# Kernel optimization log

Measured on AMD Instinct MI355X. Metric: run time of the kernel, lower is better.

The kernel has to match this reference:

```python
import jax, jax.numpy as jnp
import numpy as np

ATOM_FDIM = 133
BOND_FDIM = 147
HIDDEN = 300
DEPTH = 3
N_ATOMS = 100000
N_BONDS = 200000
MAX_NB = 6
N_MOLS = 4000


def setup_inputs() -> dict:
    key = jax.random.key(0)
    ks = jax.random.split(key, 10)
    f_atoms = jax.random.normal(ks[0], (N_ATOMS, ATOM_FDIM), dtype=jnp.float32)
    f_bonds = jax.random.normal(ks[1], (N_BONDS, BOND_FDIM), dtype=jnp.float32)
    a2b = jax.random.randint(ks[2], (N_ATOMS, MAX_NB), 0, N_BONDS)
    b2a = jax.random.randint(ks[3], (N_BONDS,), 0, N_ATOMS)
    b2revb = jax.random.randint(ks[4], (N_BONDS,), 0, N_BONDS)
    atom2mol = jnp.sort(jax.random.randint(ks[5], (N_ATOMS,), 0, N_MOLS))
    s = 1.0 / np.sqrt(HIDDEN)
    W_i = jax.random.uniform(ks[6], (BOND_FDIM, HIDDEN), jnp.float32, -s, s)
    W_h = jax.random.uniform(ks[7], (HIDDEN, HIDDEN), jnp.float32, -s, s)
    W_o_w = jax.random.uniform(ks[8], (ATOM_FDIM + HIDDEN, HIDDEN), jnp.float32, -s, s)
    W_o_b = jax.random.uniform(ks[9], (HIDDEN,), jnp.float32, -s, s)
    return {"f_atoms": f_atoms, "f_bonds": f_bonds, "a2b": a2b, "b2a": b2a,
            "b2revb": b2revb, "atom2mol": atom2mol, "W_i": W_i, "W_h": W_h,
            "W_o_w": W_o_w, "W_o_b": W_o_b}


def reference(f_atoms, f_bonds, a2b, b2a, b2revb, atom2mol, W_i, W_h, W_o_w, W_o_b):
    # input = W_i(f_bonds); message = act(input)
    inp = f_bonds @ W_i                      # [n_bonds, hidden]
    message = jax.nn.relu(inp)
    for _ in range(DEPTH - 1):
        # gather neighbor bond messages per atom and sum: [n_atoms, max_nb, h] -> [n_atoms, h]
        a_message = message[a2b].sum(axis=1)
        rev_message = message[b2revb]        # [n_bonds, hidden]
        message = a_message[b2a] - rev_message
        message = jax.nn.relu(inp + message @ W_h)
    # final atom-level aggregation
    a_message = message[a2b].sum(axis=1)     # [n_atoms, hidden]
    a_input = jnp.concatenate([f_atoms, a_message], axis=1)
    atom_hiddens = jax.nn.relu(a_input @ W_o_w + W_o_b)
    # segment mean pooling over molecules
    sums = jax.ops.segment_sum(atom_hiddens, atom2mol, num_segments=N_MOLS)
    counts = jax.ops.segment_sum(jnp.ones((atom_hiddens.shape[0],), atom_hiddens.dtype),
                                 atom2mol, num_segments=N_MOLS)
    mol_vecs = sums / jnp.maximum(counts, 1.0)[:, None]  # zero vec for empty mols
    return mol_vecs
```

## Files before the change

### kernel.cpp

```cpp
#include <hip/hip_runtime.h>
#include <stdint.h>

#define ATOM_FDIM 133
#define BOND_FDIM 147
#define HIDDEN    300
#define N_ATOMS   100000
#define N_BONDS   200000
#define MAX_NB    6
#define N_MOLS    4000

#define KP_I 160
#define KP_H 320
#define KP_O 448
#define LDA  304
#define CPR  38

#define TM   128
#define ACH  8
#define BCH  20

typedef unsigned short u16;
typedef short bf16x8 __attribute__((ext_vector_type(8)));
typedef float f32x4 __attribute__((ext_vector_type(4)));

__device__ __forceinline__ u16 f2bu(float f) {
    unsigned u = __float_as_uint(f);
    u += 0x7FFFu + ((u >> 16) & 1u);
    return (u16)(u >> 16);
}
__device__ __forceinline__ float bu2f(u16 b) { return __uint_as_float(((unsigned)b) << 16); }

__device__ __forceinline__ uint4 relu_bf16x8(uint4 v) {
    union { uint4 u; u16 s[8]; } x, o;
    x.u = v;
    #pragma unroll
    for (int e = 0; e < 8; ++e) o.s[e] = (x.s[e] & 0x8000u) ? (u16)0 : x.s[e];
    return o.u;
}
__device__ __forceinline__ uint4 comb_bf16x8(uint4 vi, uint4 va, uint4 vy) {
    union { uint4 u; u16 s[8]; } xi, xa, xy, o;
    xi.u = vi; xa.u = va; xy.u = vy;
    #pragma unroll
    for (int e = 0; e < 8; ++e)
        o.s[e] = f2bu(fmaxf(bu2f(xi.s[e]) + bu2f(xa.s[e]) - bu2f(xy.s[e]), 0.f));
    return o.u;
}

#define AS1 __attribute__((address_space(1)))
#define AS3 __attribute__((address_space(3)))
__device__ __forceinline__ void gl_lds(const void* g, void* l) {
    __builtin_amdgcn_global_load_lds((const AS1 void*)g, (AS3 void*)l, 16, 0, 0);
}

template <int EPI>
__global__ __launch_bounds__(512, 2) void mm_k(
    const u16* __restrict__ A, int lda,
    const u16* __restrict__ Wp,
    const float* __restrict__ bias,
    u16* __restrict__ out0, int ldo0,
    int M, int NT)
{
    __shared__ __align__(16) u16 As[3][ACH * 512];
    __shared__ __align__(16) u16 Bs[3][BCH * 512];

    const int t    = threadIdx.x;
    const int lane = t & 63, wid = t >> 6;
    const int fl   = lane & 15, fh = lane >> 4;
    const int m0   = blockIdx.x * TM;
    const int wr   = wid >> 1, wc = wid & 1;

    int arow = m0 + wid * 16 + fl;
    if (arow > M - 1) arow = M - 1;
    const char* srcAp = (const char*)A + (size_t)arow * (size_t)lda * 2u + (size_t)(fh * 16);
    const char* WpC = (const char*)Wp;
    const int bbase = (wid < 4) ? 3 * wid : 12 + 2 * (wid - 4);
    const size_t srcB0 = (size_t)bbase * 1024u + (size_t)lane * 16u;

    f32x4 acc[2][10] = {};

#define STAGE_T(kt, buf) do {                                                    \
        const size_t kbB_ = (size_t)(kt) * (size_t)(BCH * 1024);                 \
        gl_lds(srcAp + (size_t)(kt) * 64u, (char*)As[buf] + wid * 1024);         \
        gl_lds(WpC + kbB_ + srcB0,        (char*)Bs[buf] + bbase * 1024);        \
        gl_lds(WpC + kbB_ + srcB0 + 1024, (char*)Bs[buf] + bbase * 1024 + 1024); \
        if (wid < 4)                                                             \
            gl_lds(WpC + kbB_ + srcB0 + 2048, (char*)Bs[buf] + bbase * 1024 + 2048); \
    } while (0)

#define GATE() do {                                                        \
        if (wid < 4) asm volatile("s_waitcnt vmcnt(4)" ::: "memory");      \
        else         asm volatile("s_waitcnt vmcnt(3)" ::: "memory");      \
    } while (0)

    STAGE_T(0, 0);
    STAGE_T(1, 1);
    GATE();
    __builtin_amdgcn_s_barrier();

    int cur = 0;
    for (int tt = 0; tt < NT; ++tt) {
        int w2 = tt + 2; if (w2 >= NT) w2 -= NT;
        const int nx1 = (cur < 2) ? cur + 1 : 0;
        const int nx2 = (nx1 < 2) ? nx1 + 1 : 0;
        const u16* as_c = As[cur];
        const u16* bs_c = Bs[cur];
        const size_t kbB = (size_t)w2 * (size_t)(BCH * 1024);

        bf16x8 af0, af1, bfv[10];
        af0 = *reinterpret_cast<const bf16x8*>(&as_c[(wr * 2 + 0) * 512 + lane * 8]);
        af1 = *reinterpret_cast<const bf16x8*>(&as_c[(wr * 2 + 1) * 512 + lane * 8]);
        #pragma unroll
        for (int n = 0; n < 5; ++n)
            bfv[n] = *reinterpret_cast<const bf16x8*>(&bs_c[(wc * 10 + n) * 512 + lane * 8]);
        gl_lds(srcAp + (size_t)w2 * 64u, (char*)As[nx2] + wid * 1024);
        gl_lds(WpC + kbB + srcB0, (char*)Bs[nx2] + bbase * 1024);
        __builtin_amdgcn_s_barrier();
        __builtin_amdgcn_s_setprio(1);
        #pragma unroll
        for (int n = 0; n < 5; ++n) {
            acc[0][n] = __builtin_amdgcn_mfma_f32_16x16x32_bf16(af0, bfv[n], acc[0][n], 0, 0, 0);
            acc[1][n] = __builtin_amdgcn_mfma_f32_16x16x32_bf16(af1, bfv[n], acc[1][n], 0, 0, 0);
        }
        __builtin_amdgcn_s_setprio(0);
        __builtin_amdgcn_s_barrier();

        #pragma unroll
        for (int n = 5; n < 10; ++n)
            bfv[n] = *reinterpret_cast<const bf16x8*>(&bs_c[(wc * 10 + n) * 512 + lane * 8]);
        gl_lds(WpC + kbB + srcB0 + 1024, (char*)Bs[nx2] + bbase * 1024 + 1024);
        if (wid < 4)
            gl_lds(WpC + kbB + srcB0 + 2048, (char*)Bs[nx2] + bbase * 1024 + 2048);
        GATE();
        __builtin_amdgcn_s_barrier();
        __builtin_amdgcn_s_setprio(1);
        #pragma unroll
        for (int n = 5; n < 10; ++n) {
            acc[0][n] = __builtin_amdgcn_mfma_f32_16x16x32_bf16(af0, bfv[n], acc[0][n], 0, 0, 0);
            acc[1][n] = __builtin_amdgcn_mfma_f32_16x16x32_bf16(af1, bfv[n], acc[1][n], 0, 0, 0);
        }
        __builtin_amdgcn_s_setprio(0);
        __builtin_amdgcn_s_barrier();
        cur = nx1;
    }
#undef STAGE_T
#undef GATE

    #pragma unroll
    for (int m = 0; m < 2; ++m) {
        #pragma unroll
        for (int r = 0; r < 4; ++r) {
            const int row = m0 + wr * 32 + m * 16 + fh * 4 + r;
            if (row >= M) continue;
            #pragma unroll
            for (int n = 0; n < 10; ++n) {
                const int col = wc * 160 + n * 16 + fl;
                if (col >= HIDDEN) continue;
                const float v = acc[m][n][r];
                if (EPI == 1) out0[(size_t)row * ldo0 + col] = f2bu(v);
                else          out0[(size_t)row * ldo0 + col] = f2bu(fmaxf(v + bias[col], 0.f));
            }
        }
    }
}

template <int AM>
__global__ __launch_bounds__(512, 2) void mmf_k(
    const u16* __restrict__ A, int lda,
    const u16* __restrict__ aYp,
    const u16* __restrict__ Yp,
    const int* __restrict__ b2a,
    const int* __restrict__ b2revb,
    const u16* __restrict__ Wp,
    u16* __restrict__ out0, int ldo0,
    int M, int NT)
{
    __shared__ __align__(16) u16 As[2][ACH * 512];
    __shared__ __align__(16) u16 Bs[3][BCH * 512];

    const int t    = threadIdx.x;
    const int lane = t & 63, wid = t >> 6;
    const int fl   = lane & 15, fh = lane >> 4;
    const int m0   = blockIdx.x * TM;
    const int wr   = wid >> 1, wc = wid & 1;

    int arow = m0 + wid * 16 + fl;
    if (arow > M - 1) arow = M - 1;
    const char* pI = (const char*)A + (size_t)arow * (size_t)lda * 2u + (size_t)(fh * 16);
    const char* pA = nullptr; const char* pY = nullptr;
    if constexpr (AM == 2) {
        const int ia = b2a[arow], ir = b2revb[arow];
        pA = (const char*)aYp + (size_t)ia * (LDA * 2) + (size_t)(fh * 16);
        pY = (const char*)Yp  + (size_t)ir * (LDA * 2) + (size_t)(fh * 16);
    }
    const char* WpC = (const char*)Wp;
    const int bbase = (wid < 4) ? 3 * wid : 12 + 2 * (wid - 4);
    const size_t srcB0 = (size_t)bbase * 1024u + (size_t)lane * 16u;

    f32x4 acc[2][10] = {};
    uint4 Xi, Xa, Xy, Yi, Ya, Yy;
    (void)Xa; (void)Xy; (void)Ya; (void)Yy;

    Xi = *reinterpret_cast<const uint4*>(pI);
    if constexpr (AM == 2) { Xa = *reinterpret_cast<const uint4*>(pA);
                             Xy = *reinterpret_cast<const uint4*>(pY); }
    gl_lds(WpC + srcB0, (char*)Bs[0] + bbase * 1024);
    gl_lds(WpC + srcB0 + 1024, (char*)Bs[0] + bbase * 1024 + 1024);
    if (wid < 4) gl_lds(WpC + srcB0 + 2048, (char*)Bs[0] + bbase * 1024 + 2048);
    Yi = *reinterpret_cast<const uint4*>(pI + 64);
    if constexpr (AM == 2) { Ya = *reinterpret_cast<const uint4*>(pA + 64);
                             Yy = *reinterpret_cast<const uint4*>(pY + 64); }
    {
        const size_t kb1 = (size_t)(BCH * 1024);
        gl_lds(WpC + kb1 + srcB0, (char*)Bs[1] + bbase * 1024);
        gl_lds(WpC + kb1 + srcB0 + 1024, (char*)Bs[1] + bbase * 1024 + 1024);
        if (wid < 4) gl_lds(WpC + kb1 + srcB0 + 2048, (char*)Bs[1] + bbase * 1024 + 2048);
    }
    if constexpr (AM == 2) {
        if (wid < 4) asm volatile("s_waitcnt vmcnt(9)" ::: "memory");
        else         asm volatile("s_waitcnt vmcnt(7)" ::: "memory");
    } else {
        if (wid < 4) asm volatile("s_waitcnt vmcnt(7)" ::: "memory");
        else         asm volatile("s_waitcnt vmcnt(5)" ::: "memory");
    }
    {
        uint4 w0;
        if constexpr (AM == 2) w0 = comb_bf16x8(Xi, Xa, Xy);
        else                   w0 = relu_bf16x8(Xi);
        *reinterpret_cast<uint4*>(&As[0][wid * 512 + lane * 8]) = w0;
    }
    if constexpr (AM == 2) {
        if (wid < 4) asm volatile("s_waitcnt vmcnt(6)" ::: "memory");
        else         asm volatile("s_waitcnt vmcnt(5)" ::: "memory");
    } else {
        if (wid < 4) asm volatile("s_waitcnt vmcnt(4)" ::: "memory");
        else         asm volatile("s_waitcnt vmcnt(3)" ::: "memory");
    }
    asm volatile("s_waitcnt lgkmcnt(0)" ::: "memory");
    __builtin_amdgcn_s_barrier();

    int tt = 0, bcur = 0;

#define GATE() do {                                                        \
    if constexpr (AM == 2) {                                               \
        if (wid < 4) asm volatile("s_waitcnt vmcnt(6)" ::: "memory");      \
        else         asm volatile("s_waitcnt vmcnt(5)" ::: "memory");      \
    } else {                                                               \
        if (wid < 4) asm volatile("s_waitcnt vmcnt(4)" ::: "memory");      \
        else         asm volatile("s_waitcnt vmcnt(3)" ::: "memory");      \
    } } while (0)

#define STEP(LI, LA, LY, WI, WA, WY) do {                                                   \
    int w2 = tt + 2; if (w2 >= NT) w2 -= NT;                                                \
    const u16* as_c = As[tt & 1];                                                           \
    const u16* bs_c = Bs[bcur];                                                             \
    int bnx = bcur + 2; if (bnx >= 3) bnx -= 3;                                             \
    char* bdst = (char*)Bs[bnx] + bbase * 1024;                                             \
    const size_t kbB = (size_t)w2 * (size_t)(BCH * 1024);                                   \
    bf16x8 af0, af1, bfv[10];                                                               \
    af0 = *reinterpret_cast<const bf16x8*>(&as_c[(wr * 2 + 0) * 512 + lane * 8]);           \
    af1 = *reinterpret_cast<const bf16x8*>(&as_c[(wr * 2 + 1) * 512 + lane * 8]);           \
    _Pragma("unroll")                                                                       \
    for (int n = 0; n < 5; ++n)                                                             \
        bfv[n] = *reinterpret_cast<const bf16x8*>(&bs_c[(wc * 10 + n) * 512 + lane * 8]);   \
    LI = *reinterpret_cast<const uint4*>(pI + (size_t)w2 * 64u);                            \
    if constexpr (AM == 2) {                                                                \
        LA = *reinterpret_cast<const uint4*>(pA + (size_t)w2 * 64u);                        \
        LY = *reinterpret_cast<const uint4*>(pY + (size_t)w2 * 64u);                        \
    }                                                                                       \
    gl_lds(WpC + kbB + srcB0, bdst);                                                        \
    __builtin_amdgcn_s_barrier();                                                           \
    __builtin_amdgcn_s_setprio(1);                                                          \
    _Pragma("unroll")                                                                       \
    for (int n = 0; n < 5; ++n) {                                                           \
        acc[0][n] = __builtin_amdgcn_mfma_f32_16x16x32_bf16(af0, bfv[n], acc[0][n], 0,0,0); \
        acc[1][n] = __builtin_amdgcn_mfma_f32_16x16x32_bf16(af1, bfv[n], acc[1][n], 0,0,0); \
    }                                                                                       \
    __builtin_amdgcn_s_setprio(0);                                                          \
    __builtin_amdgcn_s_barrier();                                                           \
    _Pragma("unroll")                                                                       \
    for (int n = 5; n < 10; ++n)                                                            \
        bfv[n] = *reinterpret_cast<const bf16x8*>(&bs_c[(wc * 10 + n) * 512 + lane * 8]);   \
    gl_lds(WpC + kbB + srcB0 + 1024, bdst + 1024);                                          \
    if (wid < 4) gl_lds(WpC + kbB + srcB0 + 2048, bdst + 2048);                             \
    GATE();                                                                                 \
    {                                                                                       \
        uint4 wv;                                                                           \
        if constexpr (AM == 2) wv = comb_bf16x8(WI, WA, WY);                                \
        else                   wv = relu_bf16x8(WI);                                        \
        *reinterpret_cast<uint4*>(&As[(tt + 1) & 1][wid * 512 + lane * 8]) = wv;            \
    }                                                                                       \
    asm volatile("s_waitcnt lgkmcnt(0)" ::: "memory");                                      \
    __builtin_amdgcn_s_barrier();                                                           \
    __builtin_amdgcn_s_setprio(1);                                                          \
    _Pragma("unroll")                                                                       \
    for (int n = 5; n < 10; ++n) {                                                          \
        acc[0][n] = __builtin_amdgcn_mfma_f32_16x16x32_bf16(af0, bfv[n], acc[0][n], 0,0,0); \
        acc[1][n] = __builtin_amdgcn_mfma_f32_16x16x32_bf16(af1, bfv[n], acc[1][n], 0,0,0); \
    }                                                                                       \
    __builtin_amdgcn_s_setprio(0);                                                          \
    __builtin_amdgcn_s_barrier();                                                           \
    ++tt; bcur = (bcur == 2) ? 0 : bcur + 1;                                                \
} while (0)

    while (tt + 1 < NT) {
        STEP(Xi, Xa, Xy, Yi, Ya, Yy);
        STEP(Yi, Ya, Yy, Xi, Xa, Xy);
    }
    if (tt < NT) STEP(Xi, Xa, Xy, Yi, Ya, Yy);
#undef STEP
#undef GATE

    #pragma unroll
    for (int m = 0; m < 2; ++m) {
        #pragma unroll
        for (int r = 0; r < 4; ++r) {
            const int row = m0 + wr * 32 + m * 16 + fh * 4 + r;
            if (row >= M) continue;
            #pragma unroll
            for (int n = 0; n < 10; ++n) {
                const int col = wc * 160 + n * 16 + fl;
                if (col >= HIDDEN) continue;
                out0[(size_t)row * ldo0 + col] = f2bu(acc[m][n][r]);
            }
        }
    }
}

__global__ __launch_bounds__(256) void wconv_k(const float* __restrict__ W,
                                               int split, int off1, int Ktot, int NT,
                                               u16* __restrict__ Wp)
{
    const int id = blockIdx.x * 256 + threadIdx.x;
    if (id >= NT * BCH * 512) return;
    const int block = id >> 9, rem = id & 511;
    const int l = rem >> 3, e = rem & 7;
    const int c = block % BCH, kt = block / BCH;
    const int col = c * 16 + (l & 15);
    const int k   = kt * 32 + (l >> 4) * 8 + e;
    float v = 0.f;
    if (col < HIDDEN) {
        if (k < split) {
            const int r = k + off1;
            if (r < Ktot) v = W[(size_t)r * HIDDEN + col];
        } else {
            const int r = k - split;
            if (r < off1) v = W[(size_t)r * HIDDEN + col];
        }
    }
    Wp[id] = f2bu(v);
}

__global__ __launch_bounds__(256) void fbconv_k(const float* __restrict__ fb, u16* __restrict__ dst)
{
    const int id = blockIdx.x * 256 + threadIdx.x;
    if (id >= N_BONDS * KP_I) return;
    const int r = id / KP_I, k = id - r * KP_I;
    dst[id] = f2bu(k < BOND_FDIM ? fb[(size_t)r * BOND_FDIM + k] : 0.f);
}

__global__ __launch_bounds__(256) void agg_k(const u16* __restrict__ src,
                                             const int* __restrict__ a2b,
                                             u16* __restrict__ dst)
{
    const int c = blockIdx.x * 256 + threadIdx.x;
    if (c >= N_ATOMS * CPR) return;
    const int a = c / CPR, q = c - a * CPR;
    const int h = q * 8;
    const int* nb = a2b + (size_t)a * MAX_NB;
    float s[8] = {};
    #pragma unroll
    for (int j = 0; j < MAX_NB; ++j) {
        const int r = nb[j];
        union { uint4 u; u16 s[8]; } x;
        x.u = *(const uint4*)(src + (size_t)r * LDA + h);
        #pragma unroll
        for (int e = 0; e < 8; ++e) s[e] += bu2f(x.s[e]);
    }
    union { uint4 u; u16 s[8]; } o;
    #pragma unroll
    for (int e = 0; e < 8; ++e) o.s[e] = f2bu(s[e]);
    *(uint4*)(dst + (size_t)a * LDA + h) = o.u;
}

__global__ __launch_bounds__(256) void comb_k(const u16* __restrict__ inp,
                                              const u16* __restrict__ aY,
                                              const u16* __restrict__ Y,
                                              const int* __restrict__ b2a,
                                              const int* __restrict__ b2revb,
                                              u16* __restrict__ msg)
{
    const int c = blockIdx.x * 256 + threadIdx.x;
    if (c >= N_BONDS * CPR) return;
    const int b = c / CPR, q = c - b * CPR;
    const int h = q * 8;
    const int ia = b2a[b], ir = b2revb[b];
    union { uint4 u; u16 s[8]; } xi, xa, xy, o;
    xi.u = *(const uint4*)(inp + (size_t)b * LDA + h);
    xa.u = *(const uint4*)(aY + (size_t)ia * LDA + h);
    xy.u = *(const uint4*)(Y + (size_t)ir * LDA + h);
    #pragma unroll
    for (int j = 0; j < 8; ++j)
        o.s[j] = f2bu(fmaxf(bu2f(xi.s[j]) + bu2f(xa.s[j]) - bu2f(xy.s[j]), 0.f));
    *(uint4*)(msg + (size_t)b * LDA + h) = o.u;
}

__global__ __launch_bounds__(256) void aggcat_k(const u16* __restrict__ msg,
                                                const int* __restrict__ a2b,
                                                const float* __restrict__ fa,
                                                u16* __restrict__ dst)
{
    const int id = blockIdx.x * 256 + threadIdx.x;
    if (id >= N_ATOMS * (KP_O / 4)) return;
    const int a = id / (KP_O / 4), c = id - a * (KP_O / 4);
    const int e0 = c * 4;
    union { uint2 u; u16 s[4]; } o;
    if (e0 < HIDDEN) {
        const int* nb = a2b + (size_t)a * MAX_NB;
        float s0 = 0.f, s1 = 0.f, s2 = 0.f, s3 = 0.f;
        #pragma unroll
        for (int j = 0; j < MAX_NB; ++j) {
            union { uint2 u; u16 s[4]; } x;
            x.u = *(const uint2*)(msg + (size_t)nb[j] * LDA + e0);
            s0 += bu2f(x.s[0]); s1 += bu2f(x.s[1]); s2 += bu2f(x.s[2]); s3 += bu2f(x.s[3]);
        }
        o.s[0] = f2bu(s0); o.s[1] = f2bu(s1); o.s[2] = f2bu(s2); o.s[3] = f2bu(s3);
    } else {
        #pragma unroll
        for (int j = 0; j < 4; ++j) {
            const int fi = e0 + j - HIDDEN;
            o.s[j] = (fi < ATOM_FDIM) ? f2bu(fa[(size_t)a * ATOM_FDIM + fi]) : (u16)0;
        }
    }
    *(uint2*)(dst + (size_t)a * KP_O + e0) = o.u;
}

__global__ __launch_bounds__(320) void pool_k(const u16* __restrict__ ah,
                                              const int* __restrict__ a2m,
                                              float* __restrict__ out)
{
    const int m = blockIdx.x;
    int lo, hi;
    { int l = 0, r = N_ATOMS;
      while (l < r) { int mid = (l + r) >> 1; if (a2m[mid] < m) l = mid + 1; else r = mid; }
      lo = l; }
    { int l = lo, r = N_ATOMS;
      while (l < r) { int mid = (l + r) >> 1; if (a2m[mid] < m + 1) l = mid + 1; else r = mid; }
      hi = l; }
    const float inv = 1.0f / (float)((hi - lo) > 1 ? (hi - lo) : 1);
    const int h = threadIdx.x;
    if (h >= HIDDEN) return;
    float s = 0.f;
    for (int a = lo; a < hi; ++a) s += bu2f(ah[(size_t)a * LDA + h]);
    out[(size_t)m * HIDDEN + h] = s * inv;
}

extern "C" void kernel_launch(void* const* d_in, const int* in_sizes, int n_in,
                              void* d_out, int out_size, void* d_ws, size_t ws_size,
                              hipStream_t stream)
{
    const float* f_atoms  = (const float*)d_in[0];
    const float* f_bonds  = (const float*)d_in[1];
    const int*   a2b      = (const int*)d_in[2];
    const int*   b2a      = (const int*)d_in[3];
    const int*   b2revb   = (const int*)d_in[4];
    const int*   atom2mol = (const int*)d_in[5];
    const float* W_i      = (const float*)d_in[6];
    const float* W_h      = (const float*)d_in[7];
    const float* W_o_w    = (const float*)d_in[8];
    const float* W_o_b    = (const float*)d_in[9];
    float* out = (float*)d_out;

    char* p = (char*)d_ws;
    auto alloc = [&](size_t bytes) { char* r = p; p += (bytes + 255) & ~(size_t)255; return r; };
    u16* B0 = (u16*)alloc(((size_t)N_BONDS + 16) * LDA * 2);
    u16* B1 = (u16*)alloc(((size_t)N_BONDS + 16) * LDA * 2);
    u16* B2 = (u16*)alloc(((size_t)N_BONDS + 16) * LDA * 2);
    u16* aY = (u16*)alloc(((size_t)N_ATOMS + 16) * LDA * 2);
    u16* Wpi = (u16*)alloc((size_t)(KP_I / 32) * BCH * 512 * 2);
    u16* Wph = (u16*)alloc((size_t)(KP_H / 32) * BCH * 512 * 2);
    u16* Wpo = (u16*)alloc((size_t)(KP_O / 32) * BCH * 512 * 2);
    if ((size_t)(p - (char*)d_ws) > ws_size) return;

    u16* inp    = B0;
    u16* fb16   = B1;
    u16* Y1     = B1;
    u16* Y2     = B2;
    u16* msg2   = B1;
    u16* concat = B2;
    u16* ah     = B0;

    const dim3 blk(256);
    auto g1 = [](long long n) { return dim3((unsigned)((n + 255) / 256)); };
    const dim3 blk5(512);
    const dim3 gB((N_BONDS + TM - 1) / TM);
    const dim3 gA((N_ATOMS + TM - 1) / TM);

    const int BIGSPLIT = 1 << 20;
    wconv_k<<<g1((long long)(KP_I / 32) * BCH * 512), blk, 0, stream>>>(
        W_i, BIGSPLIT, 0, BOND_FDIM, KP_I / 32, Wpi);
    wconv_k<<<g1((long long)(KP_H / 32) * BCH * 512), blk, 0, stream>>>(
        W_h, BIGSPLIT, 0, HIDDEN, KP_H / 32, Wph);
    wconv_k<<<g1((long long)(KP_O / 32) * BCH * 512), blk, 0, stream>>>(
        W_o_w, HIDDEN, ATOM_FDIM, ATOM_FDIM + HIDDEN, KP_O / 32, Wpo);
    fbconv_k<<<g1((long long)N_BONDS * KP_I), blk, 0, stream>>>(f_bonds, fb16);

    mm_k<1><<<gB, blk5, 0, stream>>>(fb16, KP_I, Wpi, nullptr,
                                     inp, LDA, N_BONDS, KP_I / 32);

    mmf_k<1><<<gB, blk5, 0, stream>>>(inp, LDA, nullptr, nullptr, nullptr, nullptr,
                                      Wph, Y1, LDA, N_BONDS, KP_H / 32);
    agg_k<<<g1((long long)N_ATOMS * CPR), blk, 0, stream>>>(Y1, a2b, aY);

    mmf_k<2><<<gB, blk5, 0, stream>>>(inp, LDA, aY, Y1, b2a, b2revb,
                                      Wph, Y2, LDA, N_BONDS, KP_H / 32);
    agg_k<<<g1((long long)N_ATOMS * CPR), blk, 0, stream>>>(Y2, a2b, aY);

    comb_k<<<g1((long long)N_BONDS * CPR), blk, 0, stream>>>(inp, aY, Y2, b2a, b2revb, msg2);
    aggcat_k<<<g1((long long)N_ATOMS * (KP_O / 4)), blk, 0, stream>>>(msg2, a2b, f_atoms, concat);

    mm_k<2><<<gA, blk5, 0, stream>>>(concat, KP_O, Wpo, W_o_b,
                                     ah, LDA, N_ATOMS, KP_O / 32);
    pool_k<<<dim3(N_MOLS), dim3(320), 0, stream>>>(ah, atom2mol, out);
}
```

Before: 840.1 us.

## Double GEMM row tile to 256 with 1024-thread blocks and simplified B staging

Raises the GEMM row tile from 128 to 256 and launches 16 waves per block, so each staged B (weight) tile is shared by twice as many rows. Each wave now stages one B chunk, plus a second for the first four waves, and all B staging is issued in one place instead of split across the two half-steps. Wait counts and buffer padding are adjusted to match, and a bounds check in the concat kernel is tightened. The cost is fewer resident blocks per CU and heavier per-block register and LDS pressure, with half as many blocks in the grid.

Result: slower. 1.138 ms (+35.5%).

```diff
diff --git a/kernel.cpp b/kernel.cpp
--- a/kernel.cpp
+++ b/kernel.cpp
@@ -15,8 +15,7 @@
 #define LDA  304
 #define CPR  38
 
-#define TM   128
-#define ACH  8
+#define TM   256
 #define BCH  20
 
 typedef unsigned short u16;
@@ -51,17 +50,18 @@
 __device__ __forceinline__ void gl_lds(const void* g, void* l) {
     __builtin_amdgcn_global_load_lds((const AS1 void*)g, (AS3 void*)l, 16, 0, 0);
 }
+#define MFMA(a, b, c) __builtin_amdgcn_mfma_f32_16x16x32_bf16((a), (b), (c), 0, 0, 0)
 
 template <int EPI>
-__global__ __launch_bounds__(512, 2) void mm_k(
+__global__ __launch_bounds__(1024) void mm_k(
     const u16* __restrict__ A, int lda,
     const u16* __restrict__ Wp,
     const float* __restrict__ bias,
     u16* __restrict__ out0, int ldo0,
     int M, int NT)
 {
-    __shared__ __align__(16) u16 As[3][ACH * 512];
-    __shared__ __align__(16) u16 Bs[3][BCH * 512];
+    __shared__ __align__(16) u16 As[3][16 * 512];
+    __shared__ __align__(16) u16 Bs[3][20 * 512];
 
     const int t    = threadIdx.x;
     const int lane = t & 63, wid = t >> 6;
@@ -73,23 +73,22 @@
     if (arow > M - 1) arow = M - 1;
     const char* srcAp = (const char*)A + (size_t)arow * (size_t)lda * 2u + (size_t)(fh * 16);
     const char* WpC = (const char*)Wp;
-    const int bbase = (wid < 4) ? 3 * wid : 12 + 2 * (wid - 4);
-    const size_t srcB0 = (size_t)bbase * 1024u + (size_t)lane * 16u;
+    const size_t srcB0 = (size_t)wid * 1024u + (size_t)lane * 16u;
+    const size_t srcB1 = (size_t)(16 + wid) * 1024u + (size_t)lane * 16u;
 
     f32x4 acc[2][10] = {};
 
-#define STAGE_T(kt, buf) do {                                                    \
-        const size_t kbB_ = (size_t)(kt) * (size_t)(BCH * 1024);                 \
-        gl_lds(srcAp + (size_t)(kt) * 64u, (char*)As[buf] + wid * 1024);         \
-        gl_lds(WpC + kbB_ + srcB0,        (char*)Bs[buf] + bbase * 1024);        \
-        gl_lds(WpC + kbB_ + srcB0 + 1024, (char*)Bs[buf] + bbase * 1024 + 1024); \
-        if (wid < 4)                                                             \
-            gl_lds(WpC + kbB_ + srcB0 + 2048, (char*)Bs[buf] + bbase * 1024 + 2048); \
+#define STAGE_T(kt, buf) do {                                                      \
+        const size_t kb_ = (size_t)(kt) * (size_t)(BCH * 1024);                    \
+        gl_lds(srcAp + (size_t)(kt) * 64u, (char*)As[buf] + wid * 1024);           \
+        gl_lds(WpC + kb_ + srcB0, (char*)Bs[buf] + wid * 1024);                    \
+        if (wid < 4)                                                               \
+            gl_lds(WpC + kb_ + srcB1, (char*)Bs[buf] + (16 + wid) * 1024);         \
     } while (0)
 
 #define GATE() do {                                                        \
-        if (wid < 4) asm volatile("s_waitcnt vmcnt(4)" ::: "memory");      \
-        else         asm volatile("s_waitcnt vmcnt(3)" ::: "memory");      \
+        if (wid < 4) asm volatile("s_waitcnt vmcnt(3)" ::: "memory");      \
+        else         asm volatile("s_waitcnt vmcnt(2)" ::: "memory");      \
     } while (0)
 
     STAGE_T(0, 0);
@@ -104,7 +103,6 @@
         const int nx2 = (nx1 < 2) ? nx1 + 1 : 0;
         const u16* as_c = As[cur];
         const u16* bs_c = Bs[cur];
-        const size_t kbB = (size_t)w2 * (size_t)(BCH * 1024);
 
         bf16x8 af0, af1, bfv[10];
         af0 = *reinterpret_cast<const bf16x8*>(&as_c[(wr * 2 + 0) * 512 + lane * 8]);
@@ -112,14 +110,13 @@
         #pragma unroll
         for (int n = 0; n < 5; ++n)
             bfv[n] = *reinterpret_cast<const bf16x8*>(&bs_c[(wc * 10 + n) * 512 + lane * 8]);
-        gl_lds(srcAp + (size_t)w2 * 64u, (char*)As[nx2] + wid * 1024);
-        gl_lds(WpC + kbB + srcB0, (char*)Bs[nx2] + bbase * 1024);
+        STAGE_T(w2, nx2);
         __builtin_amdgcn_s_barrier();
         __builtin_amdgcn_s_setprio(1);
         #pragma unroll
         for (int n = 0; n < 5; ++n) {
-            acc[0][n] = __builtin_amdgcn_mfma_f32_16x16x32_bf16(af0, bfv[n], acc[0][n], 0, 0, 0);
-            acc[1][n] = __builtin_amdgcn_mfma_f32_16x16x32_bf16(af1, bfv[n], acc[1][n], 0, 0, 0);
+            acc[0][n] = MFMA(af0, bfv[n], acc[0][n]);
+            acc[1][n] = MFMA(af1, bfv[n], acc[1][n]);
         }
         __builtin_amdgcn_s_setprio(0);
         __builtin_amdgcn_s_barrier();
@@ -127,16 +124,13 @@
         #pragma unroll
         for (int n = 5; n < 10; ++n)
             bfv[n] = *reinterpret_cast<const bf16x8*>(&bs_c[(wc * 10 + n) * 512 + lane * 8]);
-        gl_lds(WpC + kbB + srcB0 + 1024, (char*)Bs[nx2] + bbase * 1024 + 1024);
-        if (wid < 4)
-            gl_lds(WpC + kbB + srcB0 + 2048, (char*)Bs[nx2] + bbase * 1024 + 2048);
         GATE();
         __builtin_amdgcn_s_barrier();
         __builtin_amdgcn_s_setprio(1);
         #pragma unroll
         for (int n = 5; n < 10; ++n) {
-            acc[0][n] = __builtin_amdgcn_mfma_f32_16x16x32_bf16(af0, bfv[n], acc[0][n], 0, 0, 0);
-            acc[1][n] = __builtin_amdgcn_mfma_f32_16x16x32_bf16(af1, bfv[n], acc[1][n], 0, 0, 0);
+            acc[0][n] = MFMA(af0, bfv[n], acc[0][n]);
+            acc[1][n] = MFMA(af1, bfv[n], acc[1][n]);
         }
         __builtin_amdgcn_s_setprio(0);
         __builtin_amdgcn_s_barrier();
@@ -164,7 +158,7 @@
 }
 
 template <int AM>
-__global__ __launch_bounds__(512, 2) void mmf_k(
+__global__ __launch_bounds__(1024) void mmf_k(
     const u16* __restrict__ A, int lda,
     const u16* __restrict__ aYp,
     const u16* __restrict__ Yp,
@@ -174,8 +168,8 @@
     u16* __restrict__ out0, int ldo0,
     int M, int NT)
 {
-    __shared__ __align__(16) u16 As[2][ACH * 512];
-    __shared__ __align__(16) u16 Bs[3][BCH * 512];
+    __shared__ __align__(16) u16 As[2][16 * 512];
+    __shared__ __align__(16) u16 Bs[3][20 * 512];
 
     const int t    = threadIdx.x;
     const int lane = t & 63, wid = t >> 6;
@@ -193,109 +187,91 @@
         pY = (const char*)Yp  + (size_t)ir * (LDA * 2) + (size_t)(fh * 16);
     }
     const char* WpC = (const char*)Wp;
-    const int bbase = (wid < 4) ? 3 * wid : 12 + 2 * (wid - 4);
-    const size_t srcB0 = (size_t)bbase * 1024u + (size_t)lane * 16u;
+    const size_t srcB0 = (size_t)wid * 1024u + (size_t)lane * 16u;
+    const size_t srcB1 = (size_t)(16 + wid) * 1024u + (size_t)lane * 16u;
 
     f32x4 acc[2][10] = {};
     uint4 Xi, Xa, Xy, Yi, Ya, Yy;
     (void)Xa; (void)Xy; (void)Ya; (void)Yy;
 
-    Xi = *reinterpret_cast<const uint4*>(pI);
-    if constexpr (AM == 2) { Xa = *reinterpret_cast<const uint4*>(pA);
-                             Xy = *reinterpret_cast<const uint4*>(pY); }
-    gl_lds(WpC + srcB0, (char*)Bs[0] + bbase * 1024);
-    gl_lds(WpC + srcB0 + 1024, (char*)Bs[0] + bbase * 1024 + 1024);
-    if (wid < 4) gl_lds(WpC + srcB0 + 2048, (char*)Bs[0] + bbase * 1024 + 2048);
-    Yi = *reinterpret_cast<const uint4*>(pI + 64);
-    if constexpr (AM == 2) { Ya = *reinterpret_cast<const uint4*>(pA + 64);
-                             Yy = *reinterpret_cast<const uint4*>(pY + 64); }
-    {
-        const size_t kb1 = (size_t)(BCH * 1024);
-        gl_lds(WpC + kb1 + srcB0, (char*)Bs[1] + bbase * 1024);
-        gl_lds(WpC + kb1 + srcB0 + 1024, (char*)Bs[1] + bbase * 1024 + 1024);
-        if (wid < 4) gl_lds(WpC + kb1 + srcB0 + 2048, (char*)Bs[1] + bbase * 1024 + 2048);
-    }
+#define STAGE_B(kt, buf) do {                                                      \
+        const size_t kb_ = (size_t)(kt) * (size_t)(BCH * 1024);                    \
+        gl_lds(WpC + kb_ + srcB0, (char*)Bs[buf] + wid * 1024);                    \
+        if (wid < 4)                                                               \
+            gl_lds(WpC + kb_ + srcB1, (char*)Bs[buf] + (16 + wid) * 1024);         \
+    } while (0)
+#define LOADSET(kt, I0, A0, Y0) do {                                               \
+        const size_t kb_ = (size_t)(kt) * 64u;                                     \
+        I0 = *reinterpret_cast<const uint4*>(pI + kb_);                            \
+        if constexpr (AM == 2) {                                                   \
+            A0 = *reinterpret_cast<const uint4*>(pA + kb_);                        \
+            Y0 = *reinterpret_cast<const uint4*>(pY + kb_);                        \
+        }                                                                          \
+    } while (0)
+#define XF(I, Aa, Yy) (AM == 2 ? comb_bf16x8(I, Aa, Yy) : relu_bf16x8(I))
+#define GATE() do {                                                        \
+    if constexpr (AM == 2) {                                               \
+        if (wid < 4) asm volatile("s_waitcnt vmcnt(5)" ::: "memory");      \
+        else         asm volatile("s_waitcnt vmcnt(4)" ::: "memory");      \
+    } else {                                                               \
+        if (wid < 4) asm volatile("s_waitcnt vmcnt(3)" ::: "memory");      \
+        else         asm volatile("s_waitcnt vmcnt(2)" ::: "memory");      \
+    } } while (0)
+
+    LOADSET(0, Xi, Xa, Xy);
+    STAGE_B(0, 0);
+    LOADSET(1, Yi, Ya, Yy);
+    STAGE_B(1, 1);
     if constexpr (AM == 2) {
-        if (wid < 4) asm volatile("s_waitcnt vmcnt(9)" ::: "memory");
-        else         asm volatile("s_waitcnt vmcnt(7)" ::: "memory");
-    } else {
         if (wid < 4) asm volatile("s_waitcnt vmcnt(7)" ::: "memory");
         else         asm volatile("s_waitcnt vmcnt(5)" ::: "memory");
-    }
-    {
-        uint4 w0;
-        if constexpr (AM == 2) w0 = comb_bf16x8(Xi, Xa, Xy);
-        else                   w0 = relu_bf16x8(Xi);
-        *reinterpret_cast<uint4*>(&As[0][wid * 512 + lane * 8]) = w0;
-    }
-    if constexpr (AM == 2) {
-        if (wid < 4) asm volatile("s_waitcnt vmcnt(6)" ::: "memory");
-        else         asm volatile("s_waitcnt vmcnt(5)" ::: "memory");
     } else {
-        if (wid < 4) asm volatile("s_waitcnt vmcnt(4)" ::: "memory");
+        if (wid < 4) asm volatile("s_waitcnt vmcnt(5)" ::: "memory");
         else         asm volatile("s_waitcnt vmcnt(3)" ::: "memory");
     }
+    *reinterpret_cast<uint4*>(&As[0][wid * 512 + lane * 8]) = XF(Xi, Xa, Xy);
+    GATE();
     asm volatile("s_waitcnt lgkmcnt(0)" ::: "memory");
     __builtin_amdgcn_s_barrier();
 
     int tt = 0, bcur = 0;
-
-#define GATE() do {                                                        \
-    if constexpr (AM == 2) {                                               \
-        if (wid < 4) asm volatile("s_waitcnt vmcnt(6)" ::: "memory");      \
-        else         asm volatile("s_waitcnt vmcnt(5)" ::: "memory");      \
-    } else {                                                               \
-        if (wid < 4) asm volatile("s_waitcnt vmcnt(4)" ::: "memory");      \
-        else         asm volatile("s_waitcnt vmcnt(3)" ::: "memory");      \
-    } } while (0)
 
 #define STEP(LI, LA, LY, WI, WA, WY) do {                                                   \
     int w2 = tt + 2; if (w2 >= NT) w2 -= NT;                                                \
     const u16* as_c = As[tt & 1];                                                           \
     const u16* bs_c = Bs[bcur];                                                             \
     int bnx = bcur + 2; if (bnx >= 3) bnx -= 3;                                             \
-    char* bdst = (char*)Bs[bnx] + bbase * 1024;                                             \
-    const size_t kbB = (size_t)w2 * (size_t)(BCH * 1024);                                   \
     bf16x8 af0, af1, bfv[10];                                                               \
+                                                                               \
     af0 = *reinterpret_cast<const bf16x8*>(&as_c[(wr * 2 + 0) * 512 + lane * 8]);           \
     af1 = *reinterpret_cast<const bf16x8*>(&as_c[(wr * 2 + 1) * 512 + lane * 8]);           \
     _Pragma("unroll")                                                                       \
     for (int n = 0; n < 5; ++n)                                                             \
         bfv[n] = *reinterpret_cast<const bf16x8*>(&bs_c[(wc * 10 + n) * 512 + lane * 8]);   \
-    LI = *reinterpret_cast<const uint4*>(pI + (size_t)w2 * 64u);                            \
-    if constexpr (AM == 2) {                                                                \
-        LA = *reinterpret_cast<const uint4*>(pA + (size_t)w2 * 64u);                        \
-        LY = *reinterpret_cast<const uint4*>(pY + (size_t)w2 * 64u);                        \
-    }                                                                                       \
-    gl_lds(WpC + kbB + srcB0, bdst);                                                        \
+    STAGE_B(w2, bnx);                                                                       \
+    LOADSET(w2, LI, LA, LY);                                                                \
     __builtin_amdgcn_s_barrier();                                                           \
     __builtin_amdgcn_s_setprio(1);                                                          \
     _Pragma("unroll")                                                                       \
     for (int n = 0; n < 5; ++n) {                                                           \
-        acc[0][n] = __builtin_amdgcn_mfma_f32_16x16x32_bf16(af0, bfv[n], acc[0][n], 0,0,0); \
-        acc[1][n] = __builtin_amdgcn_mfma_f32_16x16x32_bf16(af1, bfv[n], acc[1][n], 0,0,0); \
+        acc[0][n] = MFMA(af0, bfv[n], acc[0][n]);                                           \
+        acc[1][n] = MFMA(af1, bfv[n], acc[1][n]);                                           \
     }                                                                                       \
     __builtin_amdgcn_s_setprio(0);                                                          \
     __builtin_amdgcn_s_barrier();                                                           \
+                                                                               \
     _Pragma("unroll")                                                                       \
     for (int n = 5; n < 10; ++n)                                                            \
         bfv[n] = *reinterpret_cast<const bf16x8*>(&bs_c[(wc * 10 + n) * 512 + lane * 8]);   \
-    gl_lds(WpC + kbB + srcB0 + 1024, bdst + 1024);                                          \
-    if (wid < 4) gl_lds(WpC + kbB + srcB0 + 2048, bdst + 2048);                             \
-    GATE();                                                                                 \
-    {                                                                                       \
-        uint4 wv;                                                                           \
-        if constexpr (AM == 2) wv = comb_bf16x8(WI, WA, WY);                                \
-        else                   wv = relu_bf16x8(WI);                                        \
-        *reinterpret_cast<uint4*>(&As[(tt + 1) & 1][wid * 512 + lane * 8]) = wv;            \
-    }                                                                                       \
+    GATE();                                               \
+    *reinterpret_cast<uint4*>(&As[(tt + 1) & 1][wid * 512 + lane * 8]) = XF(WI, WA, WY);    \
     asm volatile("s_waitcnt lgkmcnt(0)" ::: "memory");                                      \
     __builtin_amdgcn_s_barrier();                                                           \
     __builtin_amdgcn_s_setprio(1);                                                          \
     _Pragma("unroll")                                                                       \
     for (int n = 5; n < 10; ++n) {                                                          \
-        acc[0][n] = __builtin_amdgcn_mfma_f32_16x16x32_bf16(af0, bfv[n], acc[0][n], 0,0,0); \
-        acc[1][n] = __builtin_amdgcn_mfma_f32_16x16x32_bf16(af1, bfv[n], acc[1][n], 0,0,0); \
+        acc[0][n] = MFMA(af0, bfv[n], acc[0][n]);                                           \
+        acc[1][n] = MFMA(af1, bfv[n], acc[1][n]);                                           \
     }                                                                                       \
     __builtin_amdgcn_s_setprio(0);                                                          \
     __builtin_amdgcn_s_barrier();                                                           \
@@ -308,6 +284,9 @@
     }
     if (tt < NT) STEP(Xi, Xa, Xy, Yi, Ya, Yy);
 #undef STEP
+#undef LOADSET
+#undef STAGE_B
+#undef XF
 #undef GATE
 
     #pragma unroll
@@ -327,11 +306,11 @@
 }
 
 __global__ __launch_bounds__(256) void wconv_k(const float* __restrict__ W,
-                                               int split, int off1, int Ktot, int NT,
+                                               int split, int off1, int Ktot, int NT32,
                                                u16* __restrict__ Wp)
 {
     const int id = blockIdx.x * 256 + threadIdx.x;
-    if (id >= NT * BCH * 512) return;
+    if (id >= NT32 * BCH * 512) return;
     const int block = id >> 9, rem = id & 511;
     const int l = rem >> 3, e = rem & 7;
     const int c = block % BCH, kt = block / BCH;
@@ -428,7 +407,7 @@
         #pragma unroll
         for (int j = 0; j < 4; ++j) {
             const int fi = e0 + j - HIDDEN;
-            o.s[j] = (fi < ATOM_FDIM) ? f2bu(fa[(size_t)a * ATOM_FDIM + fi]) : (u16)0;
+            o.s[j] = (fi >= 0 && fi < ATOM_FDIM) ? f2bu(fa[(size_t)a * ATOM_FDIM + fi]) : (u16)0;
         }
     }
     *(uint2*)(dst + (size_t)a * KP_O + e0) = o.u;
@@ -472,10 +451,10 @@
 
     char* p = (char*)d_ws;
     auto alloc = [&](size_t bytes) { char* r = p; p += (bytes + 255) & ~(size_t)255; return r; };
-    u16* B0 = (u16*)alloc(((size_t)N_BONDS + 16) * LDA * 2);
-    u16* B1 = (u16*)alloc(((size_t)N_BONDS + 16) * LDA * 2);
-    u16* B2 = (u16*)alloc(((size_t)N_BONDS + 16) * LDA * 2);
-    u16* aY = (u16*)alloc(((size_t)N_ATOMS + 16) * LDA * 2);
+    u16* B0 = (u16*)alloc(((size_t)N_BONDS + TM) * LDA * 2);
+    u16* B1 = (u16*)alloc(((size_t)N_BONDS + TM) * LDA * 2);
+    u16* B2 = (u16*)alloc(((size_t)N_BONDS + TM) * LDA * 2);
+    u16* aY = (u16*)alloc(((size_t)N_ATOMS + TM) * LDA * 2);
     u16* Wpi = (u16*)alloc((size_t)(KP_I / 32) * BCH * 512 * 2);
     u16* Wph = (u16*)alloc((size_t)(KP_H / 32) * BCH * 512 * 2);
     u16* Wpo = (u16*)alloc((size_t)(KP_O / 32) * BCH * 512 * 2);
@@ -491,7 +470,7 @@
 
     const dim3 blk(256);
     auto g1 = [](long long n) { return dim3((unsigned)((n + 255) / 256)); };
-    const dim3 blk5(512);
+    const dim3 blkG(1024);
     const dim3 gB((N_BONDS + TM - 1) / TM);
     const dim3 gA((N_ATOMS + TM - 1) / TM);
 
@@ -504,21 +483,21 @@
         W_o_w, HIDDEN, ATOM_FDIM, ATOM_FDIM + HIDDEN, KP_O / 32, Wpo);
     fbconv_k<<<g1((long long)N_BONDS * KP_I), blk, 0, stream>>>(f_bonds, fb16);
 
-    mm_k<1><<<gB, blk5, 0, stream>>>(fb16, KP_I, Wpi, nullptr,
+    mm_k<1><<<gB, blkG, 0, stream>>>(fb16, KP_I, Wpi, nullptr,
                                      inp, LDA, N_BONDS, KP_I / 32);
 
-    mmf_k<1><<<gB, blk5, 0, stream>>>(inp, LDA, nullptr, nullptr, nullptr, nullptr,
+    mmf_k<1><<<gB, blkG, 0, stream>>>(inp, LDA, nullptr, nullptr, nullptr, nullptr,
                                       Wph, Y1, LDA, N_BONDS, KP_H / 32);
     agg_k<<<g1((long long)N_ATOMS * CPR), blk, 0, stream>>>(Y1, a2b, aY);
 
-    mmf_k<2><<<gB, blk5, 0, stream>>>(inp, LDA, aY, Y1, b2a, b2revb,
+    mmf_k<2><<<gB, blkG, 0, stream>>>(inp, LDA, aY, Y1, b2a, b2revb,
                                       Wph, Y2, LDA, N_BONDS, KP_H / 32);
     agg_k<<<g1((long long)N_ATOMS * CPR), blk, 0, stream>>>(Y2, a2b, aY);
 
     comb_k<<<g1((long long)N_BONDS * CPR), blk, 0, stream>>>(inp, aY, Y2, b2a, b2revb, msg2);
     aggcat_k<<<g1((long long)N_ATOMS * (KP_O / 4)), blk, 0, stream>>>(msg2, a2b, f_atoms, concat);
 
-    mm_k<2><<<gA, blk5, 0, stream>>>(concat, KP_O, Wpo, W_o_b,
+    mm_k<2><<<gA, blkG, 0, stream>>>(concat, KP_O, Wpo, W_o_b,
                                      ah, LDA, N_ATOMS, KP_O / 32);
     pool_k<<<dim3(N_MOLS), dim3(320), 0, stream>>>(ah, atom2mol, out);
 }
```
